# Optimization experiments

Measured on AMD Instinct MI355X. Metric: run time of the kernel, lower is better.

## Reference

```python
import math
import jax, jax.numpy as jnp
import numpy as np

C = 256; H = 8; L = 6; F = 1024; NL = 4; P = 4; NC = 80; B = 8; Q = 300
SHAPES = [(80, 80), (40, 40), (20, 20), (10, 10)]
S = sum(h * w for h, w in SHAPES)
HEAD_DIM = C // H


def layer_norm(x, g, b, eps=1e-5):
    m = x.mean(-1, keepdims=True)
    v = ((x - m) ** 2).mean(-1, keepdims=True)
    return (x - m) * jax.lax.rsqrt(v + eps) * g + b


def inverse_sigmoid(x, eps=1e-5):
    x = jnp.clip(x, 0.0, 1.0)
    return jnp.log(jnp.clip(x, eps, None)) - jnp.log(jnp.clip(1.0 - x, eps, None))


def sine_pos_embed(pos, num_feats, temperature=10000.0):
    # pos: [B,Q,4] -> [B,Q,4*num_feats], interleaved sin/cos per coordinate
    scale = 2.0 * math.pi
    dim_t = temperature ** (2.0 * (jnp.arange(num_feats) // 2).astype(jnp.float32) / num_feats)
    x = pos[..., None] * scale / dim_t  # [B,Q,4,num_feats]
    emb = jnp.stack([jnp.sin(x[..., 0::2]), jnp.cos(x[..., 1::2])], axis=-1)
    emb = emb.reshape(x.shape[:-1] + (num_feats,))
    return emb.reshape(pos.shape[0], pos.shape[1], -1)


def mha(x, Wqkv, bqkv, Wo, bo):
    Bq, Qq, Cq = x.shape
    q, k, v = jnp.split(x @ Wqkv + bqkv, 3, axis=-1)
    q = q.reshape(Bq, Qq, H, HEAD_DIM)
    k = k.reshape(Bq, Qq, H, HEAD_DIM)
    v = v.reshape(Bq, Qq, H, HEAD_DIM)
    att = jax.nn.softmax(jnp.einsum('bqhd,bkhd->bhqk', q, k) / math.sqrt(HEAD_DIM), axis=-1)
    return jnp.einsum('bhqk,bkhd->bqhd', att, v).reshape(Bq, Qq, Cq) @ Wo + bo


def msda(value, shapes_np, starts_np, loc, attn_w):
    # value [B,S,H,D]; loc [B,Q,H,NL,P,2] in [0,1]; attn_w [B,Q,H,NL,P]
    # grid_sample semantics: align_corners=False, zero padding
    Bv, Sv, Hv, Dv = value.shape
    Qv, Pv = loc.shape[1], loc.shape[4]
    acc = jnp.zeros((Bv, Hv, Qv, Dv), value.dtype)
    for lvl in range(shapes_np.shape[0]):
        Hl, Wl = int(shapes_np[lvl, 0]), int(shapes_np[lvl, 1])
        st = int(starts_np[lvl])
        v = jnp.transpose(value[:, st:st + Hl * Wl], (0, 2, 1, 3))  # [B,H,HW,D]
        l = loc[:, :, :, lvl]  # [B,Q,H,P,2]
        x = l[..., 0] * Wl - 0.5
        y = l[..., 1] * Hl - 0.5
        x0 = jnp.floor(x); y0 = jnp.floor(y)
        fx = x - x0; fy = y - y0
        samp = jnp.zeros((Bv, Hv, Qv, Pv, Dv), value.dtype)
        for dy in (0, 1):
            for dx in (0, 1):
                xi = x0 + dx; yi = y0 + dy
                w = (fx if dx else 1.0 - fx) * (fy if dy else 1.0 - fy)
                valid = (xi >= 0) & (xi < Wl) & (yi >= 0) & (yi < Hl)
                w = jnp.where(valid, w, 0.0)  # [B,Q,H,P]
                idx = (jnp.clip(yi, 0, Hl - 1) * Wl + jnp.clip(xi, 0, Wl - 1)).astype(jnp.int32)
                idx = jnp.transpose(idx, (0, 2, 1, 3)).reshape(Bv, Hv, Qv * Pv, 1)
                g = jnp.take_along_axis(v, jnp.broadcast_to(idx, (Bv, Hv, Qv * Pv, Dv)), axis=2)
                samp = samp + g.reshape(Bv, Hv, Qv, Pv, Dv) * jnp.transpose(w, (0, 2, 1, 3))[..., None]
        aw = jnp.transpose(attn_w[:, :, :, lvl], (0, 2, 1, 3))  # [B,H,Q,P]
        acc = acc + (samp * aw[..., None]).sum(3)
    return jnp.transpose(acc, (0, 2, 1, 3)).reshape(Bv, Qv, Hv * Dv)


def _forward(fl, shapes_np, starts_np):
    (target, rpu, memory, valid_ratios,
     sa_Wqkv, sa_bqkv, sa_Wo, sa_bo,
     ca_Woff, ca_boff, ca_Wattn, ca_battn, ca_Wv, ca_bv, ca_Wout, ca_bout,
     ffn_W1, ffn_b1, ffn_W2, ffn_b2,
     ln1_g, ln1_b, ln2_g, ln2_b, ln3_g, ln3_b,
     norm_g, norm_b, qpos_W1, qpos_b1, qpos_W2, qpos_b2,
     cls_W, cls_b, box_W1, box_b1, box_W2, box_b2, box_W3, box_b3) = fl
    ref = jax.nn.sigmoid(rpu)  # [B,Q,4]
    vr4 = jnp.tile(valid_ratios, (1, 1, 2))  # [B,NL,4]
    output = target
    boxes, logits = [], []
    for i in range(L):
        ref_in = ref[:, :, None, :] * vr4[:, None]  # [B,Q,NL,4]
        qsrc = ref_in[..., 0, :]  # [B,Q,4]
        pe = sine_pos_embed(qsrc, C // 2)  # [B,Q,2C]
        qpos = jax.nn.relu(pe @ qpos_W1 + qpos_b1) @ qpos_W2 + qpos_b2
        # self attention
        q = output + qpos
        sa = mha(q, sa_Wqkv[i], sa_bqkv[i], sa_Wo[i], sa_bo[i])
        output = layer_norm(output + sa, ln1_g[i], ln1_b[i])
        # deformable cross attention
        q = output + qpos
        off = (q @ ca_Woff[i] + ca_boff[i]).reshape(B, Q, H, NL, P, 2)
        aw = jax.nn.softmax((q @ ca_Wattn[i] + ca_battn[i]).reshape(B, Q, H, NL * P), -1).reshape(B, Q, H, NL, P)
        val = (memory @ ca_Wv[i] + ca_bv[i]).reshape(B, S, H, HEAD_DIM)
        loc = ref_in[:, :, None, :, None, :2] + off / P * ref_in[:, :, None, :, None, 2:] * 0.5
        ca = msda(val, shapes_np, starts_np, loc, aw) @ ca_Wout[i] + ca_bout[i]
        output = layer_norm(output + ca, ln2_g[i], ln2_b[i])
        # FFN
        ffn = jax.nn.relu(output @ ffn_W1[i] + ffn_b1[i]) @ ffn_W2[i] + ffn_b2[i]
        output = layer_norm(output + ffn, ln3_g[i], ln3_b[i])
        # heads
        no = layer_norm(output, norm_g, norm_b)
        bh = jax.nn.relu(no @ box_W1[i] + box_b1[i])
        bh = jax.nn.relu(bh @ box_W2[i] + box_b2[i])
        pred_boxes = jax.nn.sigmoid(bh @ box_W3[i] + box_b3[i] + inverse_sigmoid(ref))
        pred_logits = no @ cls_W[i] + cls_b[i]
        boxes.append(pred_boxes)
        logits.append(pred_logits)
        ref = pred_boxes  # eval mode: no detach
    return jnp.stack(boxes), jnp.stack(logits)


def setup_inputs():
    key = jax.random.key(0)
    ks = [jax.random.fold_in(key, i) for i in range(64)]
    ki = iter(ks)
    def nrm(shape, s=0.05):
        return jax.random.normal(next(ki), shape, dtype=jnp.float32) * s
    starts = np.cumsum([0] + [h * w for h, w in SHAPES])[:-1]
    return dict(
        target=nrm((B, Q, C), 1.0),
        reference_points_unact=nrm((B, Q, 4), 1.0),
        memory=nrm((B, S, C), 1.0),
        valid_ratios=jnp.ones((B, NL, 2), jnp.float32),
        sa_Wqkv=nrm((L, C, 3 * C)), sa_bqkv=jnp.zeros((L, 3 * C)),
        sa_Wo=nrm((L, C, C)), sa_bo=jnp.zeros((L, C)),
        ca_Woff=nrm((L, C, H * NL * P * 2), 0.01), ca_boff=nrm((L, H * NL * P * 2), 0.1),
        ca_Wattn=nrm((L, C, H * NL * P)), ca_battn=jnp.zeros((L, H * NL * P)),
        ca_Wv=nrm((L, C, C)), ca_bv=jnp.zeros((L, C)),
        ca_Wout=nrm((L, C, C)), ca_bout=jnp.zeros((L, C)),
        ffn_W1=nrm((L, C, F)), ffn_b1=jnp.zeros((L, F)),
        ffn_W2=nrm((L, F, C)), ffn_b2=jnp.zeros((L, C)),
        ln1_g=jnp.ones((L, C)), ln1_b=jnp.zeros((L, C)),
        ln2_g=jnp.ones((L, C)), ln2_b=jnp.zeros((L, C)),
        ln3_g=jnp.ones((L, C)), ln3_b=jnp.zeros((L, C)),
        norm_g=jnp.ones((C,)), norm_b=jnp.zeros((C,)),
        qpos_W1=nrm((2 * C, C)), qpos_b1=jnp.zeros((C,)),
        qpos_W2=nrm((C, C)), qpos_b2=jnp.zeros((C,)),
        cls_W=nrm((L, C, NC)), cls_b=jnp.zeros((L, NC)),
        box_W1=nrm((L, C, C)), box_b1=jnp.zeros((L, C)),
        box_W2=nrm((L, C, C)), box_b2=jnp.zeros((L, C)),
        box_W3=nrm((L, C, 4)), box_b3=jnp.zeros((L, 4)),
        spatial_shapes=jnp.array(SHAPES, jnp.int32),
        level_start_index=jnp.array(starts, jnp.int32),
    )


def reference(target, reference_points_unact, memory, valid_ratios,
              sa_Wqkv, sa_bqkv, sa_Wo, sa_bo,
              ca_Woff, ca_boff, ca_Wattn, ca_battn, ca_Wv, ca_bv, ca_Wout, ca_bout,
              ffn_W1, ffn_b1, ffn_W2, ffn_b2,
              ln1_g, ln1_b, ln2_g, ln2_b, ln3_g, ln3_b,
              norm_g, norm_b, qpos_W1, qpos_b1, qpos_W2, qpos_b2,
              cls_W, cls_b, box_W1, box_b1, box_W2, box_b2, box_W3, box_b3,
              spatial_shapes, level_start_index):
    shapes_np = np.asarray(spatial_shapes)
    starts_np = np.asarray(level_start_index)
    fl = (target, reference_points_unact, memory, valid_ratios,
          sa_Wqkv, sa_bqkv, sa_Wo, sa_bo,
          ca_Woff, ca_boff, ca_Wattn, ca_battn, ca_Wv, ca_bv, ca_Wout, ca_bout,
          ffn_W1, ffn_b1, ffn_W2, ffn_b2,
          ln1_g, ln1_b, ln2_g, ln2_b, ln3_g, ln3_b,
          norm_g, norm_b, qpos_W1, qpos_b1, qpos_W2, qpos_b2,
          cls_W, cls_b, box_W1, box_b1, box_W2, box_b2, box_W3, box_b3)
    return _forward(fl, shapes_np, starts_np)
```

## Files before the change

kernel.cpp:

```cpp
#include <hip/hip_runtime.h>


static constexpr int kB = 8, kQ = 300, kC = 256, kH = 8, kL = 6,
                     kF = 1024, kNC = 80, kS = 8500;
static constexpr int kBQ = kB * kQ;

typedef __attribute__((ext_vector_type(8))) short short8v;
typedef __attribute__((ext_vector_type(4))) float floatx4;

__device__ inline ushort f2bf(float f) {
  unsigned u = __float_as_uint(f);
  u += 0x7fff + ((u >> 16) & 1);
  return (ushort)(u >> 16);
}
__device__ inline float bf2f(ushort h) { return __uint_as_float((unsigned)h << 16); }

__global__ __launch_bounds__(256) void transpose_split_pad(
    const float* __restrict__ W, ushort* __restrict__ Whi,
    ushort* __restrict__ Wlo, int K, int N, int Npad)
{
  __shared__ float t[32][33];
  size_t matI = (size_t)blockIdx.z * K * N;
  size_t matO = (size_t)blockIdx.z * K * Npad;
  int n0 = blockIdx.x * 32, k0 = blockIdx.y * 32;
  int tx = threadIdx.x & 31, ty = threadIdx.x >> 5;
#pragma unroll
  for (int dy = 0; dy < 32; dy += 8) {
    int n = n0 + tx;
    t[ty + dy][tx] = (n < N) ? W[matI + (size_t)(k0 + ty + dy) * N + n] : 0.f;
  }
  __syncthreads();
#pragma unroll
  for (int dy = 0; dy < 32; dy += 8) {
    float v = t[tx][ty + dy];
    ushort h = f2bf(v);
    size_t o = matO + (size_t)(n0 + ty + dy) * K + k0 + tx;
    Whi[o] = h;
    Wlo[o] = f2bf(v - bf2f(h));
  }
}

__global__ __launch_bounds__(256) void gemm_x3(
    const float* __restrict__ A, const float* __restrict__ A2,
    const ushort* __restrict__ Bhi, const ushort* __restrict__ Blo,
    const float* __restrict__ bias, float* __restrict__ out,
    int M, int N, int Nout, int K, int relu)
{
  __shared__ ushort Ah[64 * 64], Al[64 * 64], Bh[64 * 64], Bl[64 * 64];
  int tid = threadIdx.x;
  int tm = blockIdx.y * 64, tn = blockIdx.x * 64;
  int lane = tid & 63, wid = tid >> 6;
  int wr = wid >> 1, wc = wid & 1;
  int lrow = lane & 15, lk = lane >> 4;
  floatx4 acc[2][2] = {};
  for (int k0 = 0; k0 < K; k0 += 64) {
#pragma unroll
    for (int it = 0; it < 2; ++it) {
      int s = tid + it * 256;
      int row = s >> 3, cphys = s & 7;
      int clog = cphys ^ (row & 7);
      int gr = tm + row; if (gr > M - 1) gr = M - 1;
      const float* gp = A + (size_t)gr * K + k0 + clog * 8;
      float4 v0 = *(const float4*)gp;
      float4 v1 = *(const float4*)(gp + 4);
      float a[8] = {v0.x, v0.y, v0.z, v0.w, v1.x, v1.y, v1.z, v1.w};
      if (A2) {
        const float* gp2 = A2 + (size_t)gr * K + k0 + clog * 8;
        float4 w0 = *(const float4*)gp2;
        float4 w1 = *(const float4*)(gp2 + 4);
        a[0] += w0.x; a[1] += w0.y; a[2] += w0.z; a[3] += w0.w;
        a[4] += w1.x; a[5] += w1.y; a[6] += w1.z; a[7] += w1.w;
      }
      ushort h[8], l[8];
#pragma unroll
      for (int j = 0; j < 8; ++j) {
        h[j] = f2bf(a[j]);
        l[j] = f2bf(a[j] - bf2f(h[j]));
      }
      *(uint4*)&Ah[s * 8] = *(const uint4*)h;
      *(uint4*)&Al[s * 8] = *(const uint4*)l;
      size_t bo = (size_t)(tn + row) * K + k0 + clog * 8;
      *(uint4*)&Bh[s * 8] = *(const uint4*)(Bhi + bo);
      *(uint4*)&Bl[s * 8] = *(const uint4*)(Blo + bo);
    }
    __syncthreads();
#pragma unroll
    for (int ks = 0; ks < 2; ++ks) {
      short8v fah[2], fal[2], fbh[2], fbl[2];
#pragma unroll
      for (int mi = 0; mi < 2; ++mi) {
        int row = wr * 32 + mi * 16 + lrow;
        int c = ks * 4 + lk;
        int p = row * 8 + (c ^ (row & 7));
        fah[mi] = *(const short8v*)&Ah[p * 8];
        fal[mi] = *(const short8v*)&Al[p * 8];
      }
#pragma unroll
      for (int ni = 0; ni < 2; ++ni) {
        int row = wc * 32 + ni * 16 + lrow;
        int c = ks * 4 + lk;
        int p = row * 8 + (c ^ (row & 7));
        fbh[ni] = *(const short8v*)&Bh[p * 8];
        fbl[ni] = *(const short8v*)&Bl[p * 8];
      }
#pragma unroll
      for (int mi = 0; mi < 2; ++mi)
#pragma unroll
        for (int ni = 0; ni < 2; ++ni) {
          acc[mi][ni] = __builtin_amdgcn_mfma_f32_16x16x32_bf16(
              fah[mi], fbh[ni], acc[mi][ni], 0, 0, 0);
          acc[mi][ni] = __builtin_amdgcn_mfma_f32_16x16x32_bf16(
              fal[mi], fbh[ni], acc[mi][ni], 0, 0, 0);
          acc[mi][ni] = __builtin_amdgcn_mfma_f32_16x16x32_bf16(
              fah[mi], fbl[ni], acc[mi][ni], 0, 0, 0);
        }
    }
    __syncthreads();
  }
#pragma unroll
  for (int mi = 0; mi < 2; ++mi) {
#pragma unroll
    for (int j = 0; j < 4; ++j) {
      int grow = tm + wr * 32 + mi * 16 + lk * 4 + j;
      if (grow >= M) continue;
#pragma unroll
      for (int ni = 0; ni < 2; ++ni) {
        int gcol = tn + wc * 32 + ni * 16 + lrow;
        if (gcol >= Nout) continue;
        float v = acc[mi][ni][j] + bias[gcol];
        if (relu) v = fmaxf(v, 0.f);
        out[(size_t)grow * Nout + gcol] = v;
      }
    }
  }
}

__global__ __launch_bounds__(256) void gemm_val(
    const float* __restrict__ A, const ushort* __restrict__ Bt,
    const float* __restrict__ bias, ushort* __restrict__ outh, int M)
{
  __shared__ ushort At[64 * 64];
  __shared__ ushort Bs[256 * 64];
  int tid = threadIdx.x;
  int tm = blockIdx.x * 64;
  int lane = tid & 63, wid = tid >> 6;
  int lrow = lane & 15, lk = lane >> 4;
  floatx4 acc[16] = {};
  for (int k0 = 0; k0 < 256; k0 += 64) {
#pragma unroll
    for (int it = 0; it < 2; ++it) {
      int s = tid + it * 256;
      int row = s >> 3, cphys = s & 7, clog = cphys ^ (row & 7);
      int gr = tm + row; if (gr > M - 1) gr = M - 1;
      const float* gp = A + (size_t)gr * 256 + k0 + clog * 8;
      float4 v0 = *(const float4*)gp;
      float4 v1 = *(const float4*)(gp + 4);
      ushort* dst = &At[s * 8];
      dst[0] = f2bf(v0.x); dst[1] = f2bf(v0.y); dst[2] = f2bf(v0.z); dst[3] = f2bf(v0.w);
      dst[4] = f2bf(v1.x); dst[5] = f2bf(v1.y); dst[6] = f2bf(v1.z); dst[7] = f2bf(v1.w);
    }
#pragma unroll
    for (int it = 0; it < 8; ++it) {
      int s = tid + it * 256;
      int row = s >> 3, cphys = s & 7, clog = cphys ^ (row & 7);
      *(uint4*)&Bs[s * 8] = *(const uint4*)(Bt + (size_t)row * 256 + k0 + clog * 8);
    }
    __syncthreads();
#pragma unroll
    for (int ks = 0; ks < 2; ++ks) {
      int c = ks * 4 + lk;
      int arow = wid * 16 + lrow;
      short8v af = *(const short8v*)&At[(arow * 8 + (c ^ (arow & 7))) * 8];
#pragma unroll
      for (int nf = 0; nf < 16; ++nf) {
        int brow = nf * 16 + lrow;
        short8v bf = *(const short8v*)&Bs[(brow * 8 + (c ^ (brow & 7))) * 8];
        acc[nf] = __builtin_amdgcn_mfma_f32_16x16x32_bf16(af, bf, acc[nf], 0, 0, 0);
      }
    }
    __syncthreads();
  }
#pragma unroll
  for (int j = 0; j < 4; ++j) {
    int grow = tm + wid * 16 + lk * 4 + j;
    if (grow >= M) continue;
#pragma unroll
    for (int nf = 0; nf < 16; ++nf) {
      int gcol = nf * 16 + lrow;
      outh[(size_t)grow * 256 + gcol] = f2bf(acc[nf][j] + bias[gcol]);
    }
  }
}

__global__ __launch_bounds__(256) void ln_kernel(
    const float* __restrict__ x, const float* __restrict__ delta,
    const float* __restrict__ g, const float* __restrict__ b,
    float* __restrict__ out)
{
  __shared__ float red[4];
  int row = blockIdx.x, t = threadIdx.x;
  size_t idx = (size_t)row * 256 + t;
  float v = x[idx] + (delta ? delta[idx] : 0.f);
  float s = v;
#pragma unroll
  for (int o = 32; o; o >>= 1) s += __shfl_xor(s, o);
  if ((t & 63) == 0) red[t >> 6] = s;
  __syncthreads();
  float mean = (red[0] + red[1] + red[2] + red[3]) * (1.f / 256.f);
  __syncthreads();
  float dv = v - mean;
  float s2 = dv * dv;
#pragma unroll
  for (int o = 32; o; o >>= 1) s2 += __shfl_xor(s2, o);
  if ((t & 63) == 0) red[t >> 6] = s2;
  __syncthreads();
  float var = (red[0] + red[1] + red[2] + red[3]) * (1.f / 256.f);
  out[idx] = dv * rsqrtf(var + 1e-5f) * g[t] + b[t];
}

__global__ void sigmoid_kernel(const float* __restrict__ x, float* __restrict__ o, int n)
{
  int i = blockIdx.x * 256 + threadIdx.x;
  if (i < n) o[i] = 1.f / (1.f + expf(-x[i]));
}

__global__ void pe_kernel(const float* __restrict__ ref, const float* __restrict__ vr,
                          float* __restrict__ pe)
{
  int idx = blockIdx.x * 256 + threadIdx.x;
  if (idx >= kBQ * 512) return;
  int ch = idx & 511, bq = idx >> 9;
  int b = bq / kQ;
  int c = ch >> 7, j = ch & 127, p = j >> 1;
  float pos = ref[bq * 4 + c] * vr[(b * 4 + 0) * 2 + (c & 1)];
  float dim = expf((float)p * (9.210340371976184f / 64.f));
  float arg = pos * 6.283185307179586f / dim;
  pe[idx] = (j & 1) ? cosf(arg) : sinf(arg);
}

__global__ __launch_bounds__(256) void attn_scores(const float* __restrict__ qkv,
                                                   float* __restrict__ sc)
{
  int bh = blockIdx.z;
  int b = bh >> 3, h = bh & 7;
  int qt = blockIdx.y * 32, kt = blockIdx.x * 32;
  __shared__ float qs[32][33], ks[32][33];
  int r = threadIdx.x >> 3, dd = (threadIdx.x & 7) * 4;
  {
    int qi = qt + r;
    float4 v = make_float4(0.f, 0.f, 0.f, 0.f);
    if (qi < kQ) v = *reinterpret_cast<const float4*>(qkv + (size_t)(b * kQ + qi) * 768 + h * 32 + dd);
    qs[r][dd] = v.x; qs[r][dd + 1] = v.y; qs[r][dd + 2] = v.z; qs[r][dd + 3] = v.w;
    int kj = kt + r;
    float4 w = make_float4(0.f, 0.f, 0.f, 0.f);
    if (kj < kQ) w = *reinterpret_cast<const float4*>(qkv + (size_t)(b * kQ + kj) * 768 + 256 + h * 32 + dd);
    ks[r][dd] = w.x; ks[r][dd + 1] = w.y; ks[r][dd + 2] = w.z; ks[r][dd + 3] = w.w;
  }
  __syncthreads();
  int ty = (threadIdx.x >> 4) * 2, tx = (threadIdx.x & 15) * 2;
  float acc[2][2] = {};
#pragma unroll
  for (int k = 0; k < 32; ++k) {
    float a0 = qs[ty][k], a1 = qs[ty + 1][k];
    float b0 = ks[tx][k], b1 = ks[tx + 1][k];
    acc[0][0] += a0 * b0; acc[0][1] += a0 * b1;
    acc[1][0] += a1 * b0; acc[1][1] += a1 * b1;
  }
  const float scale = 0.17677669529663687f;
#pragma unroll
  for (int i = 0; i < 2; ++i) {
    int qi = qt + ty + i;
    if (qi >= kQ) continue;
#pragma unroll
    for (int j = 0; j < 2; ++j) {
      int kj = kt + tx + j;
      if (kj >= kQ) continue;
      sc[((size_t)bh * kQ + qi) * kQ + kj] = acc[i][j] * scale;
    }
  }
}

__global__ __launch_bounds__(256) void softmax_rows(float* __restrict__ sc)
{
  int wid = blockIdx.x * 4 + (threadIdx.x >> 6);
  int lane = threadIdx.x & 63;
  float* row = sc + (size_t)wid * kQ;
  float v[5];
  float m = -1e30f;
#pragma unroll
  for (int i = 0; i < 5; ++i) {
    int idx = lane + i * 64;
    v[i] = (idx < kQ) ? row[idx] : -1e30f;
    m = fmaxf(m, v[i]);
  }
#pragma unroll
  for (int o = 32; o; o >>= 1) m = fmaxf(m, __shfl_xor(m, o));
  float s = 0.f;
#pragma unroll
  for (int i = 0; i < 5; ++i) { v[i] = expf(v[i] - m); s += v[i]; }
#pragma unroll
  for (int o = 32; o; o >>= 1) s += __shfl_xor(s, o);
  float inv = 1.f / s;
#pragma unroll
  for (int i = 0; i < 5; ++i) {
    int idx = lane + i * 64;
    if (idx < kQ) row[idx] = v[i] * inv;
  }
}

__global__ __launch_bounds__(256) void attn_pv(const float* __restrict__ qkv,
                                               const float* __restrict__ att,
                                               float* __restrict__ outp)
{
  int bh = blockIdx.y;
  int b = bh >> 3, h = bh & 7;
  __shared__ float vs[300][32];
  int d = threadIdx.x & 31;
  for (int k = threadIdx.x >> 5; k < kQ; k += 8)
    vs[k][d] = qkv[(size_t)(b * kQ + k) * 768 + 512 + h * 32 + d];
  __syncthreads();
  int qr = threadIdx.x >> 5;
  int qend = (kQ < (int)(blockIdx.x * 64 + 64)) ? kQ : (int)(blockIdx.x * 64 + 64);
  for (int q = blockIdx.x * 64 + qr; q < qend; q += 8) {
    const float* arow = att + ((size_t)bh * kQ + q) * kQ;
    float acc = 0.f;
    for (int k = 0; k < kQ; ++k) acc += arow[k] * vs[k][d];
    outp[(size_t)(b * kQ + q) * 256 + h * 32 + d] = acc;
  }
}

__global__ void softmax16_kernel(float* __restrict__ x)
{
  int r = blockIdx.x * 256 + threadIdx.x;
  if (r >= kBQ * kH) return;
  float* p = x + (size_t)r * 16;
  float m = -1e30f;
#pragma unroll
  for (int k = 0; k < 16; ++k) m = fmaxf(m, p[k]);
  float s = 0.f;
  float e[16];
#pragma unroll
  for (int k = 0; k < 16; ++k) { e[k] = expf(p[k] - m); s += e[k]; }
  float inv = 1.f / s;
#pragma unroll
  for (int k = 0; k < 16; ++k) p[k] = e[k] * inv;
}

__global__ __launch_bounds__(256) void msda_kernel(
    const ushort* __restrict__ val, const float* __restrict__ off,
    const float* __restrict__ aw, const float* __restrict__ ref,
    const float* __restrict__ vr, float* __restrict__ outp)
{
  int bq = blockIdx.x;
  int b = bq / kQ;
  int h = threadIdx.x >> 5, d = threadIdx.x & 31;
  const int HL[4] = {80, 40, 20, 10};
  const int ST[4] = {0, 6400, 8000, 8400};
  float r0 = ref[bq * 4 + 0], r1 = ref[bq * 4 + 1];
  float r2 = ref[bq * 4 + 2], r3 = ref[bq * 4 + 3];
  const float* offrow = off + (size_t)bq * 256 + h * 32;
  const float* awrow = aw + (size_t)bq * 128 + h * 16;
  float acc = 0.f;
#pragma unroll
  for (int l = 0; l < 4; ++l) {
    int Wl = HL[l], Hl = HL[l];
    float vrx = vr[(b * 4 + l) * 2 + 0], vry = vr[(b * 4 + l) * 2 + 1];
    float cx = r0 * vrx, cy = r1 * vry;
    float sw = r2 * vrx * 0.125f, sh = r3 * vry * 0.125f;
    const ushort* vbase = val + ((size_t)b * kS + ST[l]) * 256 + h * 32 + d;
#pragma unroll
    for (int p = 0; p < 4; ++p) {
      float ox = offrow[l * 8 + p * 2 + 0];
      float oy = offrow[l * 8 + p * 2 + 1];
      float x = (cx + ox * sw) * Wl - 0.5f;
      float y = (cy + oy * sh) * Hl - 0.5f;
      float x0f = floorf(x), y0f = floorf(y);
      int x0 = (int)x0f, y0 = (int)y0f;
      float fx = x - x0f, fy = y - y0f;
      float a = awrow[l * 4 + p];
#pragma unroll
      for (int dy = 0; dy < 2; ++dy) {
#pragma unroll
        for (int dx = 0; dx < 2; ++dx) {
          int xi = x0 + dx, yi = y0 + dy;
          if (xi < 0 || xi >= Wl || yi < 0 || yi >= Hl) continue;
          float w = (dx ? fx : 1.f - fx) * (dy ? fy : 1.f - fy);
          acc += a * w * bf2f(vbase[(size_t)(yi * Wl + xi) * 256]);
        }
      }
    }
  }
  outp[(size_t)bq * 256 + h * 32 + d] = acc;
}

__global__ void box_final(const float* __restrict__ bh2, const float* __restrict__ W3,
                          const float* __restrict__ b3, const float* __restrict__ ref,
                          float* __restrict__ outb)
{
  int i = blockIdx.x * 256 + threadIdx.x;
  if (i >= kBQ * 4) return;
  int rc = i >> 2, c = i & 3;
  const float* rowp = bh2 + (size_t)rc * 256;
  float acc = b3[c];
  for (int k = 0; k < 256; ++k) acc += rowp[k] * W3[k * 4 + c];
  float r = ref[i];
  r = fminf(fmaxf(r, 0.f), 1.f);
  float inv = logf(fmaxf(r, 1e-5f)) - logf(fmaxf(1.f - r, 1e-5f));
  outb[i] = 1.f / (1.f + expf(-(acc + inv)));
}

extern "C" void kernel_launch(void* const* d_in, const int* in_sizes, int n_in,
                              void* d_out, int out_size, void* d_ws, size_t ws_size,
                              hipStream_t stream)
{
  const float* target  = (const float*)d_in[0];
  const float* rpu     = (const float*)d_in[1];
  const float* memory  = (const float*)d_in[2];
  const float* vr      = (const float*)d_in[3];
  const float* sa_Wqkv = (const float*)d_in[4];
  const float* sa_bqkv = (const float*)d_in[5];
  const float* sa_Wo   = (const float*)d_in[6];
  const float* sa_bo   = (const float*)d_in[7];
  const float* ca_Woff = (const float*)d_in[8];
  const float* ca_boff = (const float*)d_in[9];
  const float* ca_Wattn= (const float*)d_in[10];
  const float* ca_battn= (const float*)d_in[11];
  const float* ca_Wv   = (const float*)d_in[12];
  const float* ca_bv   = (const float*)d_in[13];
  const float* ca_Wout = (const float*)d_in[14];
  const float* ca_bout = (const float*)d_in[15];
  const float* ffn_W1  = (const float*)d_in[16];
  const float* ffn_b1  = (const float*)d_in[17];
  const float* ffn_W2  = (const float*)d_in[18];
  const float* ffn_b2  = (const float*)d_in[19];
  const float* ln1_g   = (const float*)d_in[20];
  const float* ln1_b   = (const float*)d_in[21];
  const float* ln2_g   = (const float*)d_in[22];
  const float* ln2_b   = (const float*)d_in[23];
  const float* ln3_g   = (const float*)d_in[24];
  const float* ln3_b   = (const float*)d_in[25];
  const float* norm_g  = (const float*)d_in[26];
  const float* norm_b  = (const float*)d_in[27];
  const float* qpos_W1 = (const float*)d_in[28];
  const float* qpos_b1 = (const float*)d_in[29];
  const float* qpos_W2 = (const float*)d_in[30];
  const float* qpos_b2 = (const float*)d_in[31];
  const float* cls_W   = (const float*)d_in[32];
  const float* cls_b   = (const float*)d_in[33];
  const float* box_W1  = (const float*)d_in[34];
  const float* box_b1  = (const float*)d_in[35];
  const float* box_W2  = (const float*)d_in[36];
  const float* box_b2  = (const float*)d_in[37];
  const float* box_W3  = (const float*)d_in[38];
  const float* box_b3  = (const float*)d_in[39];

  char* wsb = (char*)d_ws;
  float*  pe     = (float*) (wsb + 0);
  float*  qkv    = (float*) (wsb + 4915200);
  float*  qposh  = (float*) (wsb + 12288000);
  ushort* val_bf = (ushort*)(wsb + 0);
  size_t P = 34816000;
  float*  output = (float*)(wsb + P);
  float*  qpos   = (float*)(wsb + P + 2457600);
  float*  head   = (float*)(wsb + P + 4915200);
  float*  tmp    = (float*)(wsb + P + 7372800);
  float*  offb   = (float*)(wsb + P + 9830400);
  float*  awb    = (float*)(wsb + P + 12288000);
  float*  ffnh   = (float*)(wsb + P + 13516800);
  float*  bh1    = (float*)(wsb + P + 23347200);
  float*  ref0   = (float*)(wsb + P + 25804800);
  float*  scores = (float*)(wsb + P + 25843200);
  float*  bh2 = tmp;
  float*  nob = offb;
  ushort* wHI = (ushort*)(wsb + P + 25843200 + 23040000);
  ushort* wLO = wHI + 7274496;

  ushort* wq_h    = wHI + 0,       *wq_l    = wLO + 0;
  ushort* wo_h    = wHI + 1179648, *wo_l    = wLO + 1179648;
  ushort* woff_h  = wHI + 1572864, *woff_l  = wLO + 1572864;
  ushort* wattn_h = wHI + 1966080, *wattn_l = wLO + 1966080;
  ushort* wv_h    = wHI + 2162688, *wv_l    = wLO + 2162688;
  ushort* wout_h  = wHI + 2555904, *wout_l  = wLO + 2555904;
  ushort* w1_h    = wHI + 2949120, *w1_l    = wLO + 2949120;
  ushort* w2_h    = wHI + 4521984, *w2_l    = wLO + 4521984;
  ushort* wq1_h   = wHI + 6094848, *wq1_l   = wLO + 6094848;
  ushort* wq2_h   = wHI + 6225920, *wq2_l   = wLO + 6225920;
  ushort* wb1_h   = wHI + 6291456, *wb1_l   = wLO + 6291456;
  ushort* wb2_h   = wHI + 6684672, *wb2_l   = wLO + 6684672;
  ushort* wcls_h  = wHI + 7077888, *wcls_l  = wLO + 7077888;

  transpose_split_pad<<<dim3(24, 8, 6), 256, 0, stream>>>(sa_Wqkv, wq_h, wq_l, 256, 768, 768);
  transpose_split_pad<<<dim3(8, 8, 6), 256, 0, stream>>>(sa_Wo, wo_h, wo_l, 256, 256, 256);
  transpose_split_pad<<<dim3(8, 8, 6), 256, 0, stream>>>(ca_Woff, woff_h, woff_l, 256, 256, 256);
  transpose_split_pad<<<dim3(4, 8, 6), 256, 0, stream>>>(ca_Wattn, wattn_h, wattn_l, 256, 128, 128);
  transpose_split_pad<<<dim3(8, 8, 6), 256, 0, stream>>>(ca_Wv, wv_h, wv_l, 256, 256, 256);
  transpose_split_pad<<<dim3(8, 8, 6), 256, 0, stream>>>(ca_Wout, wout_h, wout_l, 256, 256, 256);
  transpose_split_pad<<<dim3(32, 8, 6), 256, 0, stream>>>(ffn_W1, w1_h, w1_l, 256, 1024, 1024);
  transpose_split_pad<<<dim3(8, 32, 6), 256, 0, stream>>>(ffn_W2, w2_h, w2_l, 1024, 256, 256);
  transpose_split_pad<<<dim3(8, 16, 1), 256, 0, stream>>>(qpos_W1, wq1_h, wq1_l, 512, 256, 256);
  transpose_split_pad<<<dim3(8, 8, 1), 256, 0, stream>>>(qpos_W2, wq2_h, wq2_l, 256, 256, 256);
  transpose_split_pad<<<dim3(8, 8, 6), 256, 0, stream>>>(box_W1, wb1_h, wb1_l, 256, 256, 256);
  transpose_split_pad<<<dim3(8, 8, 6), 256, 0, stream>>>(box_W2, wb2_h, wb2_l, 256, 256, 256);
  transpose_split_pad<<<dim3(4, 8, 6), 256, 0, stream>>>(cls_W, wcls_h, wcls_l, 256, 80, 128);

  hipMemcpyAsync(output, target, sizeof(float) * kBQ * kC, hipMemcpyDeviceToDevice, stream);
  sigmoid_kernel<<<(kBQ * 4 + 255) / 256, 256, 0, stream>>>(rpu, ref0, kBQ * 4);

  float* boxes_out  = (float*)d_out;
  float* logits_out = (float*)d_out + kL * kBQ * 4;

  const float* ref = ref0;
  for (int i = 0; i < kL; ++i) {
    pe_kernel<<<(kBQ * 512 + 255) / 256, 256, 0, stream>>>(ref, vr, pe);
    gemm_x3<<<dim3(4, 38), 256, 0, stream>>>(pe, nullptr, wq1_h, wq1_l, qpos_b1,
                                             qposh, kBQ, 256, 256, 512, 1);
    gemm_x3<<<dim3(4, 38), 256, 0, stream>>>(qposh, nullptr, wq2_h, wq2_l, qpos_b2,
                                             qpos, kBQ, 256, 256, 256, 0);
    gemm_x3<<<dim3(12, 38), 256, 0, stream>>>(output, qpos, wq_h + (size_t)i * 196608,
                                              wq_l + (size_t)i * 196608,
                                              sa_bqkv + i * 768, qkv, kBQ, 768, 768, 256, 0);
    attn_scores<<<dim3(10, 10, 64), 256, 0, stream>>>(qkv, scores);
    softmax_rows<<<4800, 256, 0, stream>>>(scores);
    attn_pv<<<dim3(5, 64), 256, 0, stream>>>(qkv, scores, head);
    gemm_x3<<<dim3(4, 38), 256, 0, stream>>>(head, nullptr, wo_h + (size_t)i * 65536,
                                             wo_l + (size_t)i * 65536,
                                             sa_bo + i * kC, tmp, kBQ, 256, 256, 256, 0);
    ln_kernel<<<kBQ, 256, 0, stream>>>(output, tmp, ln1_g + i * kC, ln1_b + i * kC, output);
    gemm_x3<<<dim3(4, 38), 256, 0, stream>>>(output, qpos, woff_h + (size_t)i * 65536,
                                             woff_l + (size_t)i * 65536,
                                             ca_boff + i * 256, offb, kBQ, 256, 256, 256, 0);
    gemm_x3<<<dim3(2, 38), 256, 0, stream>>>(output, qpos, wattn_h + (size_t)i * 32768,
                                             wattn_l + (size_t)i * 32768,
                                             ca_battn + i * 128, awb, kBQ, 128, 128, 256, 0);
    softmax16_kernel<<<(kBQ * kH + 255) / 256, 256, 0, stream>>>(awb);
    gemm_val<<<1063, 256, 0, stream>>>(memory, wv_h + (size_t)i * 65536,
                                       ca_bv + i * kC, val_bf, kB * kS);
    msda_kernel<<<kBQ, 256, 0, stream>>>(val_bf, offb, awb, ref, vr, head);
    gemm_x3<<<dim3(4, 38), 256, 0, stream>>>(head, nullptr, wout_h + (size_t)i * 65536,
                                             wout_l + (size_t)i * 65536,
                                             ca_bout + i * kC, tmp, kBQ, 256, 256, 256, 0);
    ln_kernel<<<kBQ, 256, 0, stream>>>(output, tmp, ln2_g + i * kC, ln2_b + i * kC, output);
    gemm_x3<<<dim3(16, 38), 256, 0, stream>>>(output, nullptr, w1_h + (size_t)i * 262144,
                                              w1_l + (size_t)i * 262144,
                                              ffn_b1 + i * kF, ffnh, kBQ, kF, kF, 256, 1);
    gemm_x3<<<dim3(4, 38), 256, 0, stream>>>(ffnh, nullptr, w2_h + (size_t)i * 262144,
                                             w2_l + (size_t)i * 262144,
                                             ffn_b2 + i * kC, tmp, kBQ, 256, 256, kF, 0);
    ln_kernel<<<kBQ, 256, 0, stream>>>(output, tmp, ln3_g + i * kC, ln3_b + i * kC, output);
    ln_kernel<<<kBQ, 256, 0, stream>>>(output, nullptr, norm_g, norm_b, nob);
    gemm_x3<<<dim3(4, 38), 256, 0, stream>>>(nob, nullptr, wb1_h + (size_t)i * 65536,
                                             wb1_l + (size_t)i * 65536,
                                             box_b1 + i * kC, bh1, kBQ, 256, 256, 256, 1);
    gemm_x3<<<dim3(4, 38), 256, 0, stream>>>(bh1, nullptr, wb2_h + (size_t)i * 65536,
                                             wb2_l + (size_t)i * 65536,
                                             box_b2 + i * kC, bh2, kBQ, 256, 256, 256, 1);
    box_final<<<(kBQ * 4 + 255) / 256, 256, 0, stream>>>(bh2, box_W3 + (size_t)i * kC * 4,
                                                         box_b3 + i * 4, ref,
                                                         boxes_out + (size_t)i * kBQ * 4);
    gemm_x3<<<dim3(2, 38), 256, 0, stream>>>(nob, nullptr, wcls_h + (size_t)i * 32768,
                                             wcls_l + (size_t)i * 32768,
                                             cls_b + i * kNC,
                                             logits_out + (size_t)i * kBQ * kNC,
                                             kBQ, 128, kNC, 256, 0);
    ref = boxes_out + (size_t)i * kBQ * 4;
  }
}
```

Baseline: 2.188 ms.

## Fuse self-attention into one MFMA kernel and merge sibling GEMMs

Replaces the separate score, softmax and PV kernels with one fused attention kernel. It keeps Q, K, V and the probabilities in shared memory as fp16 and uses MFMA for both matmuls, so the full score matrix no longer goes through global memory. It also concatenates the offset and attention-weight projections into one GEMM, and the box-MLP first layer with the class head into a dual-output GEMM, which cuts launches and rereads of the input. Running the attention in fp16 instead of the previous fp32 path lowers precision.

```diff
diff --git a/kernel.cpp b/kernel.cpp
--- a/kernel.cpp
+++ b/kernel.cpp
@@ -6,6 +6,7 @@
 static constexpr int kBQ = kB * kQ;
 
 typedef __attribute__((ext_vector_type(8))) short short8v;
+typedef __attribute__((ext_vector_type(8))) _Float16 half8v;
 typedef __attribute__((ext_vector_type(4))) float floatx4;
 
 __device__ inline ushort f2bf(float f) {
@@ -15,13 +16,13 @@
 }
 __device__ inline float bf2f(ushort h) { return __uint_as_float((unsigned)h << 16); }
 
-__global__ __launch_bounds__(256) void transpose_split_pad(
+__global__ __launch_bounds__(256) void transpose_split_cat(
     const float* __restrict__ W, ushort* __restrict__ Whi,
-    ushort* __restrict__ Wlo, int K, int N, int Npad)
+    ushort* __restrict__ Wlo, int K, int N, int rowOff, int NtotRows)
 {
   __shared__ float t[32][33];
   size_t matI = (size_t)blockIdx.z * K * N;
-  size_t matO = (size_t)blockIdx.z * K * Npad;
+  size_t matO = (size_t)blockIdx.z * NtotRows * K;
   int n0 = blockIdx.x * 32, k0 = blockIdx.y * 32;
   int tx = threadIdx.x & 31, ty = threadIdx.x >> 5;
 #pragma unroll
@@ -34,10 +35,23 @@
   for (int dy = 0; dy < 32; dy += 8) {
     float v = t[tx][ty + dy];
     ushort h = f2bf(v);
-    size_t o = matO + (size_t)(n0 + ty + dy) * K + k0 + tx;
+    size_t o = matO + (size_t)(rowOff + n0 + ty + dy) * K + k0 + tx;
     Whi[o] = h;
     Wlo[o] = f2bf(v - bf2f(h));
   }
+}
+
+__global__ void concat_bias(const float* __restrict__ a, int na,
+                            const float* __restrict__ b, int nb,
+                            float* __restrict__ out, int ntot, int total)
+{
+  int i = blockIdx.x * 256 + threadIdx.x;
+  if (i >= total) return;
+  int z = i / ntot, c = i % ntot;
+  float v = 0.f;
+  if (c < na) v = a[z * na + c];
+  else if (c - na < nb) v = b[z * nb + (c - na)];
+  out[i] = v;
 }
 
 __global__ __launch_bounds__(256) void gemm_x3(
@@ -135,6 +149,97 @@
   }
 }
 
+__global__ __launch_bounds__(256) void gemm_x3_dual(
+    const float* __restrict__ A, const ushort* __restrict__ Bhi,
+    const ushort* __restrict__ Blo, const float* __restrict__ bias,
+    float* __restrict__ out1, int N1, float* __restrict__ out2, int N2,
+    int M, int K)
+{
+  __shared__ ushort Ah[64 * 64], Al[64 * 64], Bh[64 * 64], Bl[64 * 64];
+  int tid = threadIdx.x;
+  int tm = blockIdx.y * 64, tn = blockIdx.x * 64;
+  int lane = tid & 63, wid = tid >> 6;
+  int wr = wid >> 1, wc = wid & 1;
+  int lrow = lane & 15, lk = lane >> 4;
+  floatx4 acc[2][2] = {};
+  for (int k0 = 0; k0 < K; k0 += 64) {
+#pragma unroll
+    for (int it = 0; it < 2; ++it) {
+      int s = tid + it * 256;
+      int row = s >> 3, cphys = s & 7;
+      int clog = cphys ^ (row & 7);
+      int gr = tm + row; if (gr > M - 1) gr = M - 1;
+      const float* gp = A + (size_t)gr * K + k0 + clog * 8;
+      float4 v0 = *(const float4*)gp;
+      float4 v1 = *(const float4*)(gp + 4);
+      float a[8] = {v0.x, v0.y, v0.z, v0.w, v1.x, v1.y, v1.z, v1.w};
+      ushort h[8], l[8];
+#pragma unroll
+      for (int j = 0; j < 8; ++j) {
+        h[j] = f2bf(a[j]);
+        l[j] = f2bf(a[j] - bf2f(h[j]));
+      }
+      *(uint4*)&Ah[s * 8] = *(const uint4*)h;
+      *(uint4*)&Al[s * 8] = *(const uint4*)l;
+      size_t bo = (size_t)(tn + row) * K + k0 + clog * 8;
+      *(uint4*)&Bh[s * 8] = *(const uint4*)(Bhi + bo);
+      *(uint4*)&Bl[s * 8] = *(const uint4*)(Blo + bo);
+    }
+    __syncthreads();
+#pragma unroll
+    for (int ks = 0; ks < 2; ++ks) {
+      short8v fah[2], fal[2], fbh[2], fbl[2];
+#pragma unroll
+      for (int mi = 0; mi < 2; ++mi) {
+        int row = wr * 32 + mi * 16 + lrow;
+        int c = ks * 4 + lk;
+        int p = row * 8 + (c ^ (row & 7));
+        fah[mi] = *(const short8v*)&Ah[p * 8];
+        fal[mi] = *(const short8v*)&Al[p * 8];
+      }
+#pragma unroll
+      for (int ni = 0; ni < 2; ++ni) {
+        int row = wc * 32 + ni * 16 + lrow;
+        int c = ks * 4 + lk;
+        int p = row * 8 + (c ^ (row & 7));
+        fbh[ni] = *(const short8v*)&Bh[p * 8];
+        fbl[ni] = *(const short8v*)&Bl[p * 8];
+      }
+#pragma unroll
+      for (int mi = 0; mi < 2; ++mi)
+#pragma unroll
+        for (int ni = 0; ni < 2; ++ni) {
+          acc[mi][ni] = __builtin_amdgcn_mfma_f32_16x16x32_bf16(
+              fah[mi], fbh[ni], acc[mi][ni], 0, 0, 0);
+          acc[mi][ni] = __builtin_amdgcn_mfma_f32_16x16x32_bf16(
+              fal[mi], fbh[ni], acc[mi][ni], 0, 0, 0);
+          acc[mi][ni] = __builtin_amdgcn_mfma_f32_16x16x32_bf16(
+              fah[mi], fbl[ni], acc[mi][ni], 0, 0, 0);
+        }
+    }
+    __syncthreads();
+  }
+#pragma unroll
+  for (int mi = 0; mi < 2; ++mi) {
+#pragma unroll
+    for (int j = 0; j < 4; ++j) {
+      int grow = tm + wr * 32 + mi * 16 + lk * 4 + j;
+      if (grow >= M) continue;
+#pragma unroll
+      for (int ni = 0; ni < 2; ++ni) {
+        int gcol = tn + wc * 32 + ni * 16 + lrow;
+        float v = acc[mi][ni][j] + bias[gcol];
+        if (gcol < N1) {
+          out1[(size_t)grow * N1 + gcol] = fmaxf(v, 0.f);
+        } else {
+          int c2 = gcol - N1;
+          if (c2 < N2) out2[(size_t)grow * N2 + c2] = v;
+        }
+      }
+    }
+  }
+}
+
 __global__ __launch_bounds__(256) void gemm_val(
     const float* __restrict__ A, const ushort* __restrict__ Bt,
     const float* __restrict__ bias, ushort* __restrict__ outh, int M)
@@ -192,6 +297,107 @@
   }
 }
 
+__global__ __launch_bounds__(256) void attn_fused(const float* __restrict__ qkv,
+                                                  float* __restrict__ outp)
+{
+  constexpr int PST = 328;
+  __shared__ _Float16 smem[31488];
+  _Float16* Ksm  = smem;
+  _Float16* Qsm  = smem + 12160;
+  _Float16* Psm  = smem;
+  _Float16* Vtsm = smem + 20992;
+  int tid = threadIdx.x;
+  int bh = blockIdx.y, b = bh >> 3, h = bh & 7;
+  int qbase = blockIdx.x * 64;
+  int sub = tid >> 5, d = tid & 31;
+  const float qscale = 0.17677669529663687f;
+  for (int r0 = 0; r0 < 64; r0 += 8) {
+    int r = r0 + sub;
+    int qg = qbase + r; if (qg > 299) qg = 299;
+    Qsm[r * 40 + d] = (_Float16)(qkv[(size_t)(b * 300 + qg) * 768 + h * 32 + d] * qscale);
+  }
+  for (int r0 = 0; r0 < 304; r0 += 8) {
+    int r = r0 + sub;
+    int kg = (r > 299) ? 299 : r;
+    const float* base = qkv + (size_t)(b * 300 + kg) * 768 + h * 32 + d;
+    Ksm[r * 40 + d] = (_Float16)base[256];
+    Vtsm[d * PST + r] = (_Float16)((r < 300) ? base[512] : 0.f);
+  }
+  for (int i = tid; i < 32 * 24; i += 256) {
+    int dd = i / 24, c = 304 + i % 24;
+    Vtsm[dd * PST + c] = (_Float16)0.f;
+  }
+  __syncthreads();
+
+  int w = tid >> 6, l = tid & 63, lr = l & 15, lg = l >> 4;
+  floatx4 zero4 = {0.f, 0.f, 0.f, 0.f};
+  half8v qa = *(const half8v*)&Qsm[(w * 16 + lr) * 40 + lg * 8];
+  floatx4 sacc[19];
+#pragma unroll
+  for (int nt = 0; nt < 19; ++nt) {
+    half8v kb = *(const half8v*)&Ksm[(nt * 16 + lr) * 40 + lg * 8];
+    sacc[nt] = __builtin_amdgcn_mfma_f32_16x16x32_f16(qa, kb, zero4, 0, 0, 0);
+  }
+  if (lr >= 12) {
+    sacc[18][0] = -1e30f; sacc[18][1] = -1e30f;
+    sacc[18][2] = -1e30f; sacc[18][3] = -1e30f;
+  }
+  float mx[4] = {-1e30f, -1e30f, -1e30f, -1e30f};
+#pragma unroll
+  for (int nt = 0; nt < 19; ++nt)
+#pragma unroll
+    for (int j = 0; j < 4; ++j) mx[j] = fmaxf(mx[j], sacc[nt][j]);
+#pragma unroll
+  for (int off = 1; off < 16; off <<= 1)
+#pragma unroll
+    for (int j = 0; j < 4; ++j) mx[j] = fmaxf(mx[j], __shfl_xor(mx[j], off));
+  float sm[4] = {0.f, 0.f, 0.f, 0.f};
+#pragma unroll
+  for (int nt = 0; nt < 19; ++nt)
+#pragma unroll
+    for (int j = 0; j < 4; ++j) {
+      float p = __expf(sacc[nt][j] - mx[j]);
+      sacc[nt][j] = p; sm[j] += p;
+    }
+#pragma unroll
+  for (int off = 1; off < 16; off <<= 1)
+#pragma unroll
+    for (int j = 0; j < 4; ++j) sm[j] += __shfl_xor(sm[j], off);
+  float inv[4];
+#pragma unroll
+  for (int j = 0; j < 4; ++j) inv[j] = 1.f / sm[j];
+  __syncthreads();
+#pragma unroll
+  for (int nt = 0; nt < 19; ++nt)
+#pragma unroll
+    for (int j = 0; j < 4; ++j)
+      Psm[(w * 16 + lg * 4 + j) * PST + nt * 16 + lr] =
+          (_Float16)(sacc[nt][j] * inv[j]);
+  for (int i = tid; i < 64 * 24; i += 256) {
+    int rr = i / 24, c = 304 + i % 24;
+    Psm[rr * PST + c] = (_Float16)0.f;
+  }
+  __syncthreads();
+  floatx4 oacc[2] = {zero4, zero4};
+#pragma unroll
+  for (int ks = 0; ks < 10; ++ks) {
+    half8v pa = *(const half8v*)&Psm[(w * 16 + lr) * PST + ks * 32 + lg * 8];
+#pragma unroll
+    for (int dt = 0; dt < 2; ++dt) {
+      half8v vb = *(const half8v*)&Vtsm[(dt * 16 + lr) * PST + ks * 32 + lg * 8];
+      oacc[dt] = __builtin_amdgcn_mfma_f32_16x16x32_f16(pa, vb, oacc[dt], 0, 0, 0);
+    }
+  }
+#pragma unroll
+  for (int dt = 0; dt < 2; ++dt)
+#pragma unroll
+    for (int j = 0; j < 4; ++j) {
+      int qg = qbase + w * 16 + lg * 4 + j;
+      if (qg < 300)
+        outp[(size_t)(b * 300 + qg) * 256 + h * 32 + dt * 16 + lr] = oacc[dt][j];
+    }
+}
+
 __global__ __launch_bounds__(256) void ln_kernel(
     const float* __restrict__ x, const float* __restrict__ delta,
     const float* __restrict__ g, const float* __restrict__ b,
@@ -238,102 +444,12 @@
   pe[idx] = (j & 1) ? cosf(arg) : sinf(arg);
 }
 
-__global__ __launch_bounds__(256) void attn_scores(const float* __restrict__ qkv,
-                                                   float* __restrict__ sc)
-{
-  int bh = blockIdx.z;
-  int b = bh >> 3, h = bh & 7;
-  int qt = blockIdx.y * 32, kt = blockIdx.x * 32;
-  __shared__ float qs[32][33], ks[32][33];
-  int r = threadIdx.x >> 3, dd = (threadIdx.x & 7) * 4;
-  {
-    int qi = qt + r;
-    float4 v = make_float4(0.f, 0.f, 0.f, 0.f);
-    if (qi < kQ) v = *reinterpret_cast<const float4*>(qkv + (size_t)(b * kQ + qi) * 768 + h * 32 + dd);
-    qs[r][dd] = v.x; qs[r][dd + 1] = v.y; qs[r][dd + 2] = v.z; qs[r][dd + 3] = v.w;
-    int kj = kt + r;
-    float4 w = make_float4(0.f, 0.f, 0.f, 0.f);
-    if (kj < kQ) w = *reinterpret_cast<const float4*>(qkv + (size_t)(b * kQ + kj) * 768 + 256 + h * 32 + dd);
-    ks[r][dd] = w.x; ks[r][dd + 1] = w.y; ks[r][dd + 2] = w.z; ks[r][dd + 3] = w.w;
-  }
-  __syncthreads();
-  int ty = (threadIdx.x >> 4) * 2, tx = (threadIdx.x & 15) * 2;
-  float acc[2][2] = {};
-#pragma unroll
-  for (int k = 0; k < 32; ++k) {
-    float a0 = qs[ty][k], a1 = qs[ty + 1][k];
-    float b0 = ks[tx][k], b1 = ks[tx + 1][k];
-    acc[0][0] += a0 * b0; acc[0][1] += a0 * b1;
-    acc[1][0] += a1 * b0; acc[1][1] += a1 * b1;
-  }
-  const float scale = 0.17677669529663687f;
-#pragma unroll
-  for (int i = 0; i < 2; ++i) {
-    int qi = qt + ty + i;
-    if (qi >= kQ) continue;
-#pragma unroll
-    for (int j = 0; j < 2; ++j) {
-      int kj = kt + tx + j;
-      if (kj >= kQ) continue;
-      sc[((size_t)bh * kQ + qi) * kQ + kj] = acc[i][j] * scale;
-    }
-  }
-}
-
-__global__ __launch_bounds__(256) void softmax_rows(float* __restrict__ sc)
-{
-  int wid = blockIdx.x * 4 + (threadIdx.x >> 6);
-  int lane = threadIdx.x & 63;
-  float* row = sc + (size_t)wid * kQ;
-  float v[5];
-  float m = -1e30f;
-#pragma unroll
-  for (int i = 0; i < 5; ++i) {
-    int idx = lane + i * 64;
-    v[i] = (idx < kQ) ? row[idx] : -1e30f;
-    m = fmaxf(m, v[i]);
-  }
-#pragma unroll
-  for (int o = 32; o; o >>= 1) m = fmaxf(m, __shfl_xor(m, o));
-  float s = 0.f;
-#pragma unroll
-  for (int i = 0; i < 5; ++i) { v[i] = expf(v[i] - m); s += v[i]; }
-#pragma unroll
-  for (int o = 32; o; o >>= 1) s += __shfl_xor(s, o);
-  float inv = 1.f / s;
-#pragma unroll
-  for (int i = 0; i < 5; ++i) {
-    int idx = lane + i * 64;
-    if (idx < kQ) row[idx] = v[i] * inv;
-  }
-}
-
-__global__ __launch_bounds__(256) void attn_pv(const float* __restrict__ qkv,
-                                               const float* __restrict__ att,
-                                               float* __restrict__ outp)
-{
-  int bh = blockIdx.y;
-  int b = bh >> 3, h = bh & 7;
-  __shared__ float vs[300][32];
-  int d = threadIdx.x & 31;
-  for (int k = threadIdx.x >> 5; k < kQ; k += 8)
-    vs[k][d] = qkv[(size_t)(b * kQ + k) * 768 + 512 + h * 32 + d];
-  __syncthreads();
-  int qr = threadIdx.x >> 5;
-  int qend = (kQ < (int)(blockIdx.x * 64 + 64)) ? kQ : (int)(blockIdx.x * 64 + 64);
-  for (int q = blockIdx.x * 64 + qr; q < qend; q += 8) {
-    const float* arow = att + ((size_t)bh * kQ + q) * kQ;
-    float acc = 0.f;
-    for (int k = 0; k < kQ; ++k) acc += arow[k] * vs[k][d];
-    outp[(size_t)(b * kQ + q) * 256 + h * 32 + d] = acc;
-  }
-}
-
 __global__ void softmax16_kernel(float* __restrict__ x)
 {
   int r = blockIdx.x * 256 + threadIdx.x;
   if (r >= kBQ * kH) return;
-  float* p = x + (size_t)r * 16;
+  int bq = r >> 3, h = r & 7;
+  float* p = x + (size_t)bq * 384 + 256 + h * 16;
   float m = -1e30f;
 #pragma unroll
   for (int k = 0; k < 16; ++k) m = fmaxf(m, p[k]);
@@ -347,9 +463,9 @@
 }
 
 __global__ __launch_bounds__(256) void msda_kernel(
-    const ushort* __restrict__ val, const float* __restrict__ off,
-    const float* __restrict__ aw, const float* __restrict__ ref,
-    const float* __restrict__ vr, float* __restrict__ outp)
+    const ushort* __restrict__ val, const float* __restrict__ offaw,
+    const float* __restrict__ ref, const float* __restrict__ vr,
+    float* __restrict__ outp)
 {
   int bq = blockIdx.x;
   int b = bq / kQ;
@@ -358,8 +474,8 @@
   const int ST[4] = {0, 6400, 8000, 8400};
   float r0 = ref[bq * 4 + 0], r1 = ref[bq * 4 + 1];
   float r2 = ref[bq * 4 + 2], r3 = ref[bq * 4 + 3];
-  const float* offrow = off + (size_t)bq * 256 + h * 32;
-  const float* awrow = aw + (size_t)bq * 128 + h * 16;
+  const float* offrow = offaw + (size_t)bq * 384 + h * 32;
+  const float* awrow  = offaw + (size_t)bq * 384 + 256 + h * 16;
   float acc = 0.f;
 #pragma unroll
   for (int l = 0; l < 4; ++l) {
@@ -464,44 +580,44 @@
   float*  qpos   = (float*)(wsb + P + 2457600);
   float*  head   = (float*)(wsb + P + 4915200);
   float*  tmp    = (float*)(wsb + P + 7372800);
-  float*  offb   = (float*)(wsb + P + 9830400);
-  float*  awb    = (float*)(wsb + P + 12288000);
+  float*  offaw  = (float*)(wsb + P + 9830400);
   float*  ffnh   = (float*)(wsb + P + 13516800);
   float*  bh1    = (float*)(wsb + P + 23347200);
   float*  ref0   = (float*)(wsb + P + 25804800);
-  float*  scores = (float*)(wsb + P + 25843200);
+  float*  boffattn = (float*)(wsb + P + 25843200);
+  float*  bboxcls  = (float*)(wsb + P + 25852416);
   float*  bh2 = tmp;
-  float*  nob = offb;
-  ushort* wHI = (ushort*)(wsb + P + 25843200 + 23040000);
+  float*  nob = offaw;
+  ushort* wHI = (ushort*)(wsb + P + 25861632);
   ushort* wLO = wHI + 7274496;
 
   ushort* wq_h    = wHI + 0,       *wq_l    = wLO + 0;
   ushort* wo_h    = wHI + 1179648, *wo_l    = wLO + 1179648;
-  ushort* woff_h  = wHI + 1572864, *woff_l  = wLO + 1572864;
-  ushort* wattn_h = wHI + 1966080, *wattn_l = wLO + 1966080;
+  ushort* woa_h   = wHI + 1572864, *woa_l   = wLO + 1572864;
   ushort* wv_h    = wHI + 2162688, *wv_l    = wLO + 2162688;
   ushort* wout_h  = wHI + 2555904, *wout_l  = wLO + 2555904;
   ushort* w1_h    = wHI + 2949120, *w1_l    = wLO + 2949120;
   ushort* w2_h    = wHI + 4521984, *w2_l    = wLO + 4521984;
   ushort* wq1_h   = wHI + 6094848, *wq1_l   = wLO + 6094848;
   ushort* wq2_h   = wHI + 6225920, *wq2_l   = wLO + 6225920;
-  ushort* wb1_h   = wHI + 6291456, *wb1_l   = wLO + 6291456;
-  ushort* wb2_h   = wHI + 6684672, *wb2_l   = wLO + 6684672;
-  ushort* wcls_h  = wHI + 7077888, *wcls_l  = wLO + 7077888;
-
-  transpose_split_pad<<<dim3(24, 8, 6), 256, 0, stream>>>(sa_Wqkv, wq_h, wq_l, 256, 768, 768);
-  transpose_split_pad<<<dim3(8, 8, 6), 256, 0, stream>>>(sa_Wo, wo_h, wo_l, 256, 256, 256);
-  transpose_split_pad<<<dim3(8, 8, 6), 256, 0, stream>>>(ca_Woff, woff_h, woff_l, 256, 256, 256);
-  transpose_split_pad<<<dim3(4, 8, 6), 256, 0, stream>>>(ca_Wattn, wattn_h, wattn_l, 256, 128, 128);
-  transpose_split_pad<<<dim3(8, 8, 6), 256, 0, stream>>>(ca_Wv, wv_h, wv_l, 256, 256, 256);
-  transpose_split_pad<<<dim3(8, 8, 6), 256, 0, stream>>>(ca_Wout, wout_h, wout_l, 256, 256, 256);
-  transpose_split_pad<<<dim3(32, 8, 6), 256, 0, stream>>>(ffn_W1, w1_h, w1_l, 256, 1024, 1024);
-  transpose_split_pad<<<dim3(8, 32, 6), 256, 0, stream>>>(ffn_W2, w2_h, w2_l, 1024, 256, 256);
-  transpose_split_pad<<<dim3(8, 16, 1), 256, 0, stream>>>(qpos_W1, wq1_h, wq1_l, 512, 256, 256);
-  transpose_split_pad<<<dim3(8, 8, 1), 256, 0, stream>>>(qpos_W2, wq2_h, wq2_l, 256, 256, 256);
-  transpose_split_pad<<<dim3(8, 8, 6), 256, 0, stream>>>(box_W1, wb1_h, wb1_l, 256, 256, 256);
-  transpose_split_pad<<<dim3(8, 8, 6), 256, 0, stream>>>(box_W2, wb2_h, wb2_l, 256, 256, 256);
-  transpose_split_pad<<<dim3(4, 8, 6), 256, 0, stream>>>(cls_W, wcls_h, wcls_l, 256, 80, 128);
+  ushort* wbc_h   = wHI + 6291456, *wbc_l   = wLO + 6291456;
+  ushort* wb2_h   = wHI + 6881280, *wb2_l   = wLO + 6881280;
+
+  transpose_split_cat<<<dim3(24, 8, 6), 256, 0, stream>>>(sa_Wqkv, wq_h, wq_l, 256, 768, 0, 768);
+  transpose_split_cat<<<dim3(8, 8, 6), 256, 0, stream>>>(sa_Wo, wo_h, wo_l, 256, 256, 0, 256);
+  transpose_split_cat<<<dim3(8, 8, 6), 256, 0, stream>>>(ca_Woff, woa_h, woa_l, 256, 256, 0, 384);
+  transpose_split_cat<<<dim3(4, 8, 6), 256, 0, stream>>>(ca_Wattn, woa_h, woa_l, 256, 128, 256, 384);
+  transpose_split_cat<<<dim3(8, 8, 6), 256, 0, stream>>>(ca_Wv, wv_h, wv_l, 256, 256, 0, 256);
+  transpose_split_cat<<<dim3(8, 8, 6), 256, 0, stream>>>(ca_Wout, wout_h, wout_l, 256, 256, 0, 256);
+  transpose_split_cat<<<dim3(32, 8, 6), 256, 0, stream>>>(ffn_W1, w1_h, w1_l, 256, 1024, 0, 1024);
+  transpose_split_cat<<<dim3(8, 32, 6), 256, 0, stream>>>(ffn_W2, w2_h, w2_l, 1024, 256, 0, 256);
+  transpose_split_cat<<<dim3(8, 16, 1), 256, 0, stream>>>(qpos_W1, wq1_h, wq1_l, 512, 256, 0, 256);
+  transpose_split_cat<<<dim3(8, 8, 1), 256, 0, stream>>>(qpos_W2, wq2_h, wq2_l, 256, 256, 0, 256);
+  transpose_split_cat<<<dim3(8, 8, 6), 256, 0, stream>>>(box_W1, wbc_h, wbc_l, 256, 256, 0, 384);
+  transpose_split_cat<<<dim3(4, 8, 6), 256, 0, stream>>>(cls_W, wbc_h, wbc_l, 256, 80, 256, 384);
+  transpose_split_cat<<<dim3(8, 8, 6), 256, 0, stream>>>(box_W2, wb2_h, wb2_l, 256, 256, 0, 256);
+  concat_bias<<<9, 256, 0, stream>>>(ca_boff, 256, ca_battn, 128, boffattn, 384, kL * 384);
+  concat_bias<<<9, 256, 0, stream>>>(box_b1, 256, cls_b, 80, bboxcls, 384, kL * 384);
 
   hipMemcpyAsync(output, target, sizeof(float) * kBQ * kC, hipMemcpyDeviceToDevice, stream);
   sigmoid_kernel<<<(kBQ * 4 + 255) / 256, 256, 0, stream>>>(rpu, ref0, kBQ * 4);
@@ -519,23 +635,18 @@
     gemm_x3<<<dim3(12, 38), 256, 0, stream>>>(output, qpos, wq_h + (size_t)i * 196608,
                                               wq_l + (size_t)i * 196608,
                                               sa_bqkv + i * 768, qkv, kBQ, 768, 768, 256, 0);
-    attn_scores<<<dim3(10, 10, 64), 256, 0, stream>>>(qkv, scores);
-    softmax_rows<<<4800, 256, 0, stream>>>(scores);
-    attn_pv<<<dim3(5, 64), 256, 0, stream>>>(qkv, scores, head);
+    attn_fused<<<dim3(5, 64), 256, 0, stream>>>(qkv, head);
     gemm_x3<<<dim3(4, 38), 256, 0, stream>>>(head, nullptr, wo_h + (size_t)i * 65536,
                                              wo_l + (size_t)i * 65536,
                                              sa_bo + i * kC, tmp, kBQ, 256, 256, 256, 0);
     ln_kernel<<<kBQ, 256, 0, stream>>>(output, tmp, ln1_g + i * kC, ln1_b + i * kC, output);
-    gemm_x3<<<dim3(4, 38), 256, 0, stream>>>(output, qpos, woff_h + (size_t)i * 65536,
-                                             woff_l + (size_t)i * 65536,
-                                             ca_boff + i * 256, offb, kBQ, 256, 256, 256, 0);
-    gemm_x3<<<dim3(2, 38), 256, 0, stream>>>(output, qpos, wattn_h + (size_t)i * 32768,
-                                             wattn_l + (size_t)i * 32768,
-                                             ca_battn + i * 128, awb, kBQ, 128, 128, 256, 0);
-    softmax16_kernel<<<(kBQ * kH + 255) / 256, 256, 0, stream>>>(awb);
+    gemm_x3<<<dim3(6, 38), 256, 0, stream>>>(output, qpos, woa_h + (size_t)i * 98304,
+                                             woa_l + (size_t)i * 98304,
+                                             boffattn + i * 384, offaw, kBQ, 384, 384, 256, 0);
+    softmax16_kernel<<<(kBQ * kH + 255) / 256, 256, 0, stream>>>(offaw);
     gemm_val<<<1063, 256, 0, stream>>>(memory, wv_h + (size_t)i * 65536,
                                        ca_bv + i * kC, val_bf, kB * kS);
-    msda_kernel<<<kBQ, 256, 0, stream>>>(val_bf, offb, awb, ref, vr, head);
+    msda_kernel<<<kBQ, 256, 0, stream>>>(val_bf, offaw, ref, vr, head);
     gemm_x3<<<dim3(4, 38), 256, 0, stream>>>(head, nullptr, wout_h + (size_t)i * 65536,
                                              wout_l + (size_t)i * 65536,
                                              ca_bout + i * kC, tmp, kBQ, 256, 256, 256, 0);
@@ -548,20 +659,18 @@
                                              ffn_b2 + i * kC, tmp, kBQ, 256, 256, kF, 0);
     ln_kernel<<<kBQ, 256, 0, stream>>>(output, tmp, ln3_g + i * kC, ln3_b + i * kC, output);
     ln_kernel<<<kBQ, 256, 0, stream>>>(output, nullptr, norm_g, norm_b, nob);
-    gemm_x3<<<dim3(4, 38), 256, 0, stream>>>(nob, nullptr, wb1_h + (size_t)i * 65536,
-                                             wb1_l + (size_t)i * 65536,
-                                             box_b1 + i * kC, bh1, kBQ, 256, 256, 256, 1);
+    gemm_x3_dual<<<dim3(6, 38), 256, 0, stream>>>(nob, wbc_h + (size_t)i * 98304,
+                                                  wbc_l + (size_t)i * 98304,
+                                                  bboxcls + i * 384,
+                                                  bh1, 256,
+                                                  logits_out + (size_t)i * kBQ * kNC, kNC,
+                                                  kBQ, 256);
     gemm_x3<<<dim3(4, 38), 256, 0, stream>>>(bh1, nullptr, wb2_h + (size_t)i * 65536,
                                              wb2_l + (size_t)i * 65536,
                                              box_b2 + i * kC, bh2, kBQ, 256, 256, 256, 1);
     box_final<<<(kBQ * 4 + 255) / 256, 256, 0, stream>>>(bh2, box_W3 + (size_t)i * kC * 4,
                                                          box_b3 + i * 4, ref,
                                                          boxes_out + (size_t)i * kBQ * 4);
-    gemm_x3<<<dim3(2, 38), 256, 0, stream>>>(nob, nullptr, wcls_h + (size_t)i * 32768,
-                                             wcls_l + (size_t)i * 32768,
-                                             cls_b + i * kNC,
-                                             logits_out + (size_t)i * kBQ * kNC,
-                                             kBQ, 128, kNC, 256, 0);
     ref = boxes_out + (size_t)i * kBQ * 4;
   }
 }
```

New measurement: 1.803 ms. 1.21x faster.
